# Performance work log

Hardware: AMD Instinct MI355X
Metric: run time of the kernel (lower is better)

## Reference

```python
import jax, jax.numpy as jnp
import numpy as np

B, T, C = 2, 2048, 1024
N = 16
D = C // N  # 64


def setup_inputs() -> dict:
    key = jax.random.key(0)
    ks = jax.random.split(key, 5)
    s = 1.0 / np.sqrt(C)  # lecun_normal-ish scale for Dense kernels
    return {
        "src": jax.random.normal(ks[0], (B, T, C), jnp.float32),
        "mask": jnp.ones((B, T), jnp.float32),  # unused on causal path
        "Wq": jax.random.normal(ks[1], (C, C), jnp.float32) * s,
        "bq": jnp.zeros((C,), jnp.float32),
        "Wk": jax.random.normal(ks[2], (C, C), jnp.float32) * s,
        "bk": jnp.zeros((C,), jnp.float32),
        "Wv": jax.random.normal(ks[3], (C, C), jnp.float32) * s,
        "bv": jnp.zeros((C,), jnp.float32),
        "Wo": jax.random.normal(ks[4], (C, C), jnp.float32) * s,
        "bo": jnp.zeros((C,), jnp.float32),
    }


def reference(src, mask, Wq, bq, Wk, bk, Wv, bv, Wo, bo):
    # QKV projections -> [B, N, T, D]
    def heads(x):
        return x.reshape(B, T, N, D).transpose(0, 2, 1, 3)

    q = heads(src @ Wq + bq)
    k = heads(src @ Wk + bk)
    v = heads(src @ Wv + bv)

    # scores [B, N, T, T], causal mask, softmax
    scores = jnp.einsum("bntd,bnsd->bnts", q, k) / jnp.sqrt(jnp.float32(D))
    causal = jnp.tril(jnp.ones((T, T), bool))
    scores = jnp.where(causal, scores, -jnp.inf)
    attn = jax.nn.softmax(scores, axis=-1)

    # weighted values, merge heads, output projection (dropout deterministic)
    out = jnp.einsum("bnts,bnsd->bntd", attn, v)
    out = out.transpose(0, 2, 1, 3).reshape(B, T, C)
    return out @ Wo + bo
```

## Files before the change

kernel.cpp:

```cpp
#include <hip/hip_runtime.h>

typedef __bf16 bf16;
typedef bf16 bf16x8 __attribute__((ext_vector_type(8)));
typedef float f32x4 __attribute__((ext_vector_type(4)));
typedef unsigned short u16;
typedef u16 u16x4 __attribute__((ext_vector_type(4)));

typedef const __attribute__((address_space(1))) void* gptr_t;
typedef __attribute__((address_space(3))) void* sptr_t;

__device__ __forceinline__ void async16(const void* g, void* l) {
  __builtin_amdgcn_global_load_lds((gptr_t)g, (sptr_t)l, 16, 0, 0);
}
__device__ __forceinline__ u16 f2bf(float v) {
  return __builtin_bit_cast(u16, (bf16)v);
}

__global__ void kPrep(const float* __restrict__ src, u16* __restrict__ Xs,
                      const float* __restrict__ Wq, const float* __restrict__ Wk,
                      const float* __restrict__ Wv, const float* __restrict__ Wo,
                      u16* __restrict__ Wt) {
  __shared__ float tile[32][33];
  const int bid = blockIdx.x, tid = threadIdx.x;
  if (bid < 4096) {
    const int i = (bid * 256 + tid) * 4;
    float4 v = *(const float4*)&src[i];
    u16x4 o = {f2bf(v.x), f2bf(v.y), f2bf(v.z), f2bf(v.w)};
    *(u16x4*)&Xs[i] = o;
  } else {
    const int t = bid - 4096;
    const int z = t >> 10, tt = t & 1023;
    const float* W = (z == 0) ? Wq : (z == 1) ? Wk : (z == 2) ? Wv : Wo;
    const int n0 = (tt & 31) * 32, k0 = (tt >> 5) * 32;
    const int tx = tid & 31, ty = tid >> 5;
#pragma unroll
    for (int j = 0; j < 4; ++j)
      tile[ty + j * 8][tx] = W[(size_t)(k0 + ty + j * 8) * 1024 + n0 + tx];
    __syncthreads();
#pragma unroll
    for (int j = 0; j < 4; ++j)
      Wt[(size_t)z * 1048576 + (size_t)(n0 + ty + j * 8) * 1024 + k0 + tx] =
          f2bf(tile[tx][ty + j * 8]);
  }
}

template <int EPI>
__global__ __launch_bounds__(256, 2) void kGemm(
    const u16* __restrict__ A, const u16* __restrict__ Bt,
    const float* __restrict__ b0, const float* __restrict__ b1,
    const float* __restrict__ b2, u16* __restrict__ outQ,
    float* __restrict__ outF) {
  __shared__ __align__(16) u16 As[2][128 * 32];
  __shared__ __align__(16) u16 Bs[2][128 * 32];
  const int tid = threadIdx.x, l = tid & 63, w = tid >> 6;
  const int bid = (blockIdx.x & 7) * (gridDim.x >> 3) + (blockIdx.x >> 3);
  const int mb = bid & 31, nb = bid >> 5;
  const int mbase = mb * 128, nbase = nb * 128;
  const int wr = (w >> 1) * 64, wc = (w & 1) * 64;
  f32x4 acc[4][4];
#pragma unroll
  for (int i = 0; i < 4; ++i)
#pragma unroll
    for (int j = 0; j < 4; ++j) acc[i][j] = (f32x4){0.f, 0.f, 0.f, 0.f};

  auto stage = [&](int bufi, int kt) {
#pragma unroll
    for (int i = 0; i < 2; ++i) {
      const int q = (w * 2 + i) * 64 + l;
      const int r = q >> 2, sl = q & 3;
      const int ksw = (sl ^ ((r >> 1) & 3)) * 8;
      async16(&A[(size_t)(mbase + r) * 1024 + kt * 32 + ksw],
              &As[bufi][(w * 2 + i) * 512]);
      async16(&Bt[(size_t)(nbase + r) * 1024 + kt * 32 + ksw],
              &Bs[bufi][(w * 2 + i) * 512]);
    }
  };

  stage(0, 0);
  for (int kt = 0; kt < 32; ++kt) {
    const int cur = kt & 1;
    if (kt < 31) {
      stage(cur ^ 1, kt + 1);
      asm volatile("s_waitcnt vmcnt(4)" ::: "memory");
    } else {
      asm volatile("s_waitcnt vmcnt(0)" ::: "memory");
    }
    __builtin_amdgcn_s_barrier();
    __builtin_amdgcn_sched_barrier(0);

    bf16x8 a[4], b[4];
#pragma unroll
    for (int mf = 0; mf < 4; ++mf) {
      const int row = wr + mf * 16 + (l & 15);
      const int slot = (l >> 4) ^ ((row >> 1) & 3);
      a[mf] = *(const bf16x8*)&As[cur][row * 32 + slot * 8];
    }
#pragma unroll
    for (int nf = 0; nf < 4; ++nf) {
      const int row = wc + nf * 16 + (l & 15);
      const int slot = (l >> 4) ^ ((row >> 1) & 3);
      b[nf] = *(const bf16x8*)&Bs[cur][row * 32 + slot * 8];
    }
#pragma unroll
    for (int mf = 0; mf < 4; ++mf)
#pragma unroll
      for (int nf = 0; nf < 4; ++nf)
        acc[mf][nf] = __builtin_amdgcn_mfma_f32_16x16x32_bf16(a[mf], b[nf],
                                                              acc[mf][nf], 0, 0, 0);
    __builtin_amdgcn_s_barrier();
  }

  if constexpr (EPI == 0) {
    const int mat = nb >> 3;
    const float* bias = (mat == 0) ? b0 : (mat == 1) ? b1 : b2;
    const float qscale = (mat == 0) ? 0.1803368801f : 1.0f;
    u16* Qo = outQ;
    u16* Ko = outQ + 4 * 1048576;
    u16* Vo = outQ + 8 * 1048576;
#pragma unroll
    for (int nf = 0; nf < 4; ++nf) {
      const int n = nbase + wc + nf * 16 + (l & 15);
      const int c = n & 1023, h = c >> 6, d = c & 63;
      const float bsv = bias[c];
#pragma unroll
      for (int mf = 0; mf < 4; ++mf)
#pragma unroll
        for (int r = 0; r < 4; ++r) {
          const int m = mbase + wr + mf * 16 + (l >> 4) * 4 + r;
          const int bb = m >> 11, t = m & 2047;
          const u16 hv = f2bf((acc[mf][nf][r] + bsv) * qscale);
          if (mat == 0)
            Qo[((size_t)(bb * 16 + h) * 2048 + t) * 64 + d] = hv;
          else if (mat == 1)
            Ko[((size_t)(bb * 16 + h) * 2048 + t) * 64 + d] = hv;
          else
            Vo[((size_t)(bb * 16 + h) * 64 + d) * 2048 + t] = hv;
        }
    }
  } else {
#pragma unroll
    for (int nf = 0; nf < 4; ++nf) {
      const int n = nbase + wc + nf * 16 + (l & 15);
      const float bsv = b0[n];
#pragma unroll
      for (int mf = 0; mf < 4; ++mf)
#pragma unroll
        for (int r = 0; r < 4; ++r) {
          const int m = mbase + wr + mf * 16 + (l >> 4) * 4 + r;
          outF[(size_t)m * 1024 + n] = acc[mf][nf][r] + bsv;
        }
    }
  }
}

#define PSTR 88
__global__ __launch_bounds__(256, 2) void kAttn(const u16* __restrict__ Q,
                                                const u16* __restrict__ K,
                                                const u16* __restrict__ Vt,
                                                u16* __restrict__ AO) {
  __shared__ __align__(16) u16 Ksh[2][64 * 64];
  __shared__ __align__(16) u16 Vsh[2][64 * 64];
  __shared__ __align__(16) u16 Pl[4][16 * PSTR];
  const int tid = threadIdx.x, l = tid & 63, w = tid >> 6;
  const int g = l >> 4, c = l & 15;
  const int pi = blockIdx.x, bh = blockIdx.y;
  const int qtA = pi, qtB = 31 - pi;
  const size_t head = (size_t)bh * 131072;

  bf16x8 aqA[2], aqB[2];
  {
    const int qrA = qtA * 64 + w * 16 + c;
    const int qrB = qtB * 64 + w * 16 + c;
#pragma unroll
    for (int ks = 0; ks < 2; ++ks) {
      aqA[ks] = *(const bf16x8*)&Q[head + (size_t)qrA * 64 + ks * 32 + g * 8];
      aqB[ks] = *(const bf16x8*)&Q[head + (size_t)qrB * 64 + ks * 32 + g * 8];
    }
  }

  f32x4 accA[4], accB[4];
#pragma unroll
  for (int i = 0; i < 4; ++i) {
    accA[i] = (f32x4){0.f, 0.f, 0.f, 0.f};
    accB[i] = (f32x4){0.f, 0.f, 0.f, 0.f};
  }
  float lA_ = 0.f, lB_ = 0.f;

  auto stage = [&](int bufi, int st) {
#pragma unroll
    for (int i = 0; i < 2; ++i) {
      const int q = (w * 2 + i) * 64 + l;
      const int r = q >> 3, sl = q & 7;
      const int ksw = (sl ^ (r & 7)) * 8;
      async16(&K[head + (size_t)(st * 64 + r) * 64 + ksw], &Ksh[bufi][(w * 2 + i) * 512]);
      async16(&Vt[head + (size_t)r * 2048 + st * 64 + ksw], &Vsh[bufi][(w * 2 + i) * 512]);
    }
  };

  auto computeTile = [&](int st, int qt, bf16x8* aq, f32x4* accO, float& lpart,
                         int cur) {
    f32x4 sT[4];
#pragma unroll
    for (int i = 0; i < 4; ++i) sT[i] = (f32x4){0.f, 0.f, 0.f, 0.f};
#pragma unroll
    for (int ks = 0; ks < 2; ++ks)
#pragma unroll
      for (int nf = 0; nf < 4; ++nf) {
        const int row = nf * 16 + c;
        const int slot = (ks * 4 + g) ^ (row & 7);
        bf16x8 bk = *(const bf16x8*)&Ksh[cur][row * 64 + slot * 8];
        sT[nf] = __builtin_amdgcn_mfma_f32_16x16x32_bf16(bk, aq[ks], sT[nf], 0, 0, 0);
      }

    float v[16];
#pragma unroll
    for (int nf = 0; nf < 4; ++nf)
#pragma unroll
      for (int r = 0; r < 4; ++r) v[nf * 4 + r] = sT[nf][r];
    if (st == qt) {
      const int qg = w * 16 + c;
#pragma unroll
      for (int nf = 0; nf < 4; ++nf)
#pragma unroll
        for (int r = 0; r < 4; ++r)
          if (nf * 16 + g * 4 + r > qg) v[nf * 4 + r] = -__builtin_inff();
    }

    float p[16];
#pragma unroll
    for (int i = 0; i < 16; ++i) p[i] = __builtin_exp2f(v[i]);
#pragma unroll
    for (int nf = 0; nf < 4; ++nf) {
      u16x4 q4 = {f2bf(p[nf * 4 + 0]), f2bf(p[nf * 4 + 1]),
                  f2bf(p[nf * 4 + 2]), f2bf(p[nf * 4 + 3])};
      *(u16x4*)&Pl[w][c * PSTR + nf * 16 + g * 4] = q4;
    }
    float s0 = (p[0] + p[1]) + (p[2] + p[3]);
    float s1 = (p[4] + p[5]) + (p[6] + p[7]);
    float s2 = (p[8] + p[9]) + (p[10] + p[11]);
    float s3 = (p[12] + p[13]) + (p[14] + p[15]);
    lpart += (s0 + s1) + (s2 + s3);

#pragma unroll
    for (int ks2 = 0; ks2 < 2; ++ks2) {
      bf16x8 pf = *(const bf16x8*)&Pl[w][c * PSTR + ks2 * 32 + g * 8];
#pragma unroll
      for (int nd = 0; nd < 4; ++nd) {
        const int row = nd * 16 + c;
        const int slot = (ks2 * 4 + g) ^ (row & 7);
        bf16x8 vf = *(const bf16x8*)&Vsh[cur][row * 64 + slot * 8];
        accO[nd] = __builtin_amdgcn_mfma_f32_16x16x32_bf16(pf, vf, accO[nd], 0, 0, 0);
      }
    }
  };

  stage(0, 0);
  for (int st = 0; st <= qtB; ++st) {
    const int cur = st & 1;
    if (st < qtB) {
      stage(cur ^ 1, st + 1);
      asm volatile("s_waitcnt vmcnt(4)" ::: "memory");
    } else {
      asm volatile("s_waitcnt vmcnt(0)" ::: "memory");
    }
    __builtin_amdgcn_s_barrier();
    __builtin_amdgcn_sched_barrier(0);

    computeTile(st, qtB, aqB, accB, lB_, cur);
    if (st <= qtA) computeTile(st, qtA, aqA, accA, lA_, cur);

    __builtin_amdgcn_s_barrier();
  }

  const int b = bh >> 4, h = bh & 15;
  auto writeOut = [&](int qt, f32x4* accO, float lpart) {
    float lc = lpart + __shfl_xor(lpart, 16);
    lc += __shfl_xor(lc, 32);
#pragma unroll
    for (int r = 0; r < 4; ++r) {
      const float lr = __shfl(lc, g * 4 + r);
      const float rin = 1.0f / lr;
      const int t = qt * 64 + w * 16 + g * 4 + r;
#pragma unroll
      for (int nd = 0; nd < 4; ++nd)
        AO[(size_t)(b * 2048 + t) * 1024 + h * 64 + nd * 16 + c] =
            f2bf(accO[nd][r] * rin);
    }
  };
  writeOut(qtA, accA, lA_);
  writeOut(qtB, accB, lB_);
}

extern "C" void kernel_launch(void* const* d_in, const int* in_sizes, int n_in,
                              void* d_out, int out_size, void* d_ws, size_t ws_size,
                              hipStream_t stream) {
  const float* src = (const float*)d_in[0];
  const float* Wq = (const float*)d_in[2];
  const float* bq = (const float*)d_in[3];
  const float* Wk = (const float*)d_in[4];
  const float* bk = (const float*)d_in[5];
  const float* Wv = (const float*)d_in[6];
  const float* bv = (const float*)d_in[7];
  const float* Wo = (const float*)d_in[8];
  const float* bo = (const float*)d_in[9];
  float* out = (float*)d_out;

  char* ws = (char*)d_ws;
  u16* Wt = (u16*)(ws);
  u16* Xs = (u16*)(ws + 8ull * 1024 * 1024);
  u16* Qb = (u16*)(ws + 16ull * 1024 * 1024);
  u16* AO = (u16*)(ws + 40ull * 1024 * 1024);

  kPrep<<<dim3(8192), dim3(256), 0, stream>>>(src, Xs, Wq, Wk, Wv, Wo, Wt);
  kGemm<0><<<dim3(32 * 24), dim3(256), 0, stream>>>(Xs, Wt, bq, bk, bv, Qb, nullptr);
  kAttn<<<dim3(16, 32), dim3(256), 0, stream>>>(Qb, Qb + 4 * 1048576,
                                                Qb + 8 * 1048576, AO);
  kGemm<1><<<dim3(32 * 8), dim3(256), 0, stream>>>(AO, Wt + 3ull * 1048576, bo,
                                                   nullptr, nullptr, nullptr, out);
}
```

Measured before the change: 127.6 us.

## Drop LDS staging in GEMMs and attention; load MFMA operands directly from global

```diff
diff --git a/kernel.cpp b/kernel.cpp
--- a/kernel.cpp
+++ b/kernel.cpp
@@ -6,12 +6,6 @@
 typedef unsigned short u16;
 typedef u16 u16x4 __attribute__((ext_vector_type(4)));
 
-typedef const __attribute__((address_space(1))) void* gptr_t;
-typedef __attribute__((address_space(3))) void* sptr_t;
-
-__device__ __forceinline__ void async16(const void* g, void* l) {
-  __builtin_amdgcn_global_load_lds((gptr_t)g, (sptr_t)l, 16, 0, 0);
-}
 __device__ __forceinline__ u16 f2bf(float v) {
   return __builtin_bit_cast(u16, (bf16)v);
 }
@@ -44,112 +38,126 @@
   }
 }
 
-template <int EPI>
-__global__ __launch_bounds__(256, 2) void kGemm(
+__global__ __launch_bounds__(256, 2) void kGemmQKV(
     const u16* __restrict__ A, const u16* __restrict__ Bt,
     const float* __restrict__ b0, const float* __restrict__ b1,
-    const float* __restrict__ b2, u16* __restrict__ outQ,
-    float* __restrict__ outF) {
-  __shared__ __align__(16) u16 As[2][128 * 32];
-  __shared__ __align__(16) u16 Bs[2][128 * 32];
+    const float* __restrict__ b2, u16* __restrict__ outQ) {
   const int tid = threadIdx.x, l = tid & 63, w = tid >> 6;
-  const int bid = (blockIdx.x & 7) * (gridDim.x >> 3) + (blockIdx.x >> 3);
+  const int bid = (blockIdx.x & 7) * 96 + (blockIdx.x >> 3);
   const int mb = bid & 31, nb = bid >> 5;
   const int mbase = mb * 128, nbase = nb * 128;
   const int wr = (w >> 1) * 64, wc = (w & 1) * 64;
+  const int hi = l >> 4, lo = l & 15;
+
+  const u16* abase[4];
+  const u16* bbase[4];
+#pragma unroll
+  for (int mf = 0; mf < 4; ++mf)
+    abase[mf] = &A[(size_t)(mbase + wr + mf * 16 + lo) * 1024 + hi * 8];
+#pragma unroll
+  for (int nf = 0; nf < 4; ++nf)
+    bbase[nf] = &Bt[(size_t)(nbase + wc + nf * 16 + lo) * 1024 + hi * 8];
+
   f32x4 acc[4][4];
 #pragma unroll
   for (int i = 0; i < 4; ++i)
 #pragma unroll
     for (int j = 0; j < 4; ++j) acc[i][j] = (f32x4){0.f, 0.f, 0.f, 0.f};
 
-  auto stage = [&](int bufi, int kt) {
-#pragma unroll
-    for (int i = 0; i < 2; ++i) {
-      const int q = (w * 2 + i) * 64 + l;
-      const int r = q >> 2, sl = q & 3;
-      const int ksw = (sl ^ ((r >> 1) & 3)) * 8;
-      async16(&A[(size_t)(mbase + r) * 1024 + kt * 32 + ksw],
-              &As[bufi][(w * 2 + i) * 512]);
-      async16(&Bt[(size_t)(nbase + r) * 1024 + kt * 32 + ksw],
-              &Bs[bufi][(w * 2 + i) * 512]);
-    }
-  };
-
-  stage(0, 0);
+#pragma unroll 2
   for (int kt = 0; kt < 32; ++kt) {
-    const int cur = kt & 1;
-    if (kt < 31) {
-      stage(cur ^ 1, kt + 1);
-      asm volatile("s_waitcnt vmcnt(4)" ::: "memory");
-    } else {
-      asm volatile("s_waitcnt vmcnt(0)" ::: "memory");
-    }
-    __builtin_amdgcn_s_barrier();
-    __builtin_amdgcn_sched_barrier(0);
-
     bf16x8 a[4], b[4];
 #pragma unroll
-    for (int mf = 0; mf < 4; ++mf) {
-      const int row = wr + mf * 16 + (l & 15);
-      const int slot = (l >> 4) ^ ((row >> 1) & 3);
-      a[mf] = *(const bf16x8*)&As[cur][row * 32 + slot * 8];
-    }
-#pragma unroll
-    for (int nf = 0; nf < 4; ++nf) {
-      const int row = wc + nf * 16 + (l & 15);
-      const int slot = (l >> 4) ^ ((row >> 1) & 3);
-      b[nf] = *(const bf16x8*)&Bs[cur][row * 32 + slot * 8];
-    }
+    for (int mf = 0; mf < 4; ++mf) a[mf] = *(const bf16x8*)&abase[mf][kt * 32];
+#pragma unroll
+    for (int nf = 0; nf < 4; ++nf) b[nf] = *(const bf16x8*)&bbase[nf][kt * 32];
 #pragma unroll
     for (int mf = 0; mf < 4; ++mf)
 #pragma unroll
       for (int nf = 0; nf < 4; ++nf)
         acc[mf][nf] = __builtin_amdgcn_mfma_f32_16x16x32_bf16(a[mf], b[nf],
                                                               acc[mf][nf], 0, 0, 0);
-    __builtin_amdgcn_s_barrier();
-  }
-
-  if constexpr (EPI == 0) {
-    const int mat = nb >> 3;
-    const float* bias = (mat == 0) ? b0 : (mat == 1) ? b1 : b2;
-    const float qscale = (mat == 0) ? 0.1803368801f : 1.0f;
-    u16* Qo = outQ;
-    u16* Ko = outQ + 4 * 1048576;
-    u16* Vo = outQ + 8 * 1048576;
-#pragma unroll
-    for (int nf = 0; nf < 4; ++nf) {
-      const int n = nbase + wc + nf * 16 + (l & 15);
-      const int c = n & 1023, h = c >> 6, d = c & 63;
-      const float bsv = bias[c];
-#pragma unroll
-      for (int mf = 0; mf < 4; ++mf)
-#pragma unroll
-        for (int r = 0; r < 4; ++r) {
-          const int m = mbase + wr + mf * 16 + (l >> 4) * 4 + r;
-          const int bb = m >> 11, t = m & 2047;
-          const u16 hv = f2bf((acc[mf][nf][r] + bsv) * qscale);
-          if (mat == 0)
-            Qo[((size_t)(bb * 16 + h) * 2048 + t) * 64 + d] = hv;
-          else if (mat == 1)
-            Ko[((size_t)(bb * 16 + h) * 2048 + t) * 64 + d] = hv;
-          else
-            Vo[((size_t)(bb * 16 + h) * 64 + d) * 2048 + t] = hv;
-        }
-    }
-  } else {
-#pragma unroll
-    for (int nf = 0; nf < 4; ++nf) {
-      const int n = nbase + wc + nf * 16 + (l & 15);
-      const float bsv = b0[n];
-#pragma unroll
-      for (int mf = 0; mf < 4; ++mf)
-#pragma unroll
-        for (int r = 0; r < 4; ++r) {
-          const int m = mbase + wr + mf * 16 + (l >> 4) * 4 + r;
-          outF[(size_t)m * 1024 + n] = acc[mf][nf][r] + bsv;
-        }
-    }
+  }
+
+  u16* Qo = outQ;
+  u16* Ko = outQ + 4 * 1048576;
+  u16* Vo = outQ + 8 * 1048576;
+  const int mat = nb >> 3;
+  const float* bias = (mat == 0) ? b0 : (mat == 1) ? b1 : b2;
+  const float qs = (mat == 0) ? 0.1803368801f : 1.0f;
+#pragma unroll
+  for (int nf = 0; nf < 4; ++nf) {
+    const int n = nbase + wc + nf * 16 + lo;
+    const int cc = n & 1023, h = cc >> 6, d = cc & 63;
+    const float bsv = bias[cc];
+#pragma unroll
+    for (int mf = 0; mf < 4; ++mf)
+#pragma unroll
+      for (int r = 0; r < 4; ++r) {
+        const int m = mbase + wr + mf * 16 + hi * 4 + r;
+        const int bb = m >> 11, t = m & 2047;
+        const u16 hv = f2bf((acc[mf][nf][r] + bsv) * qs);
+        if (mat == 0)
+          Qo[((size_t)(bb * 16 + h) * 2048 + t) * 64 + d] = hv;
+        else if (mat == 1)
+          Ko[((size_t)(bb * 16 + h) * 2048 + t) * 64 + d] = hv;
+        else
+          Vo[((size_t)(bb * 16 + h) * 64 + d) * 2048 + t] = hv;
+      }
+  }
+}
+
+__global__ __launch_bounds__(256, 2) void kGemmO(
+    const u16* __restrict__ A, const u16* __restrict__ Bt,
+    const float* __restrict__ b0, float* __restrict__ outF) {
+  const int tid = threadIdx.x, l = tid & 63, w = tid >> 6;
+  const int bid = (blockIdx.x & 7) * 64 + (blockIdx.x >> 3);
+  const int mb = bid & 31, nb = bid >> 5;
+  const int mbase = mb * 128, nbase = nb * 64;
+  const int wr = (w >> 1) * 64, wc = (w & 1) * 32;
+  const int hi = l >> 4, lo = l & 15;
+
+  const u16* abase[4];
+  const u16* bbase[2];
+#pragma unroll
+  for (int mf = 0; mf < 4; ++mf)
+    abase[mf] = &A[(size_t)(mbase + wr + mf * 16 + lo) * 1024 + hi * 8];
+#pragma unroll
+  for (int nf = 0; nf < 2; ++nf)
+    bbase[nf] = &Bt[(size_t)(nbase + wc + nf * 16 + lo) * 1024 + hi * 8];
+
+  f32x4 acc[4][2];
+#pragma unroll
+  for (int i = 0; i < 4; ++i)
+#pragma unroll
+    for (int j = 0; j < 2; ++j) acc[i][j] = (f32x4){0.f, 0.f, 0.f, 0.f};
+
+#pragma unroll 2
+  for (int kt = 0; kt < 32; ++kt) {
+    bf16x8 a[4], b[2];
+#pragma unroll
+    for (int mf = 0; mf < 4; ++mf) a[mf] = *(const bf16x8*)&abase[mf][kt * 32];
+#pragma unroll
+    for (int nf = 0; nf < 2; ++nf) b[nf] = *(const bf16x8*)&bbase[nf][kt * 32];
+#pragma unroll
+    for (int mf = 0; mf < 4; ++mf)
+#pragma unroll
+      for (int nf = 0; nf < 2; ++nf)
+        acc[mf][nf] = __builtin_amdgcn_mfma_f32_16x16x32_bf16(a[mf], b[nf],
+                                                              acc[mf][nf], 0, 0, 0);
+  }
+
+#pragma unroll
+  for (int nf = 0; nf < 2; ++nf) {
+    const int n = nbase + wc + nf * 16 + lo;
+    const float bsv = b0[n];
+#pragma unroll
+    for (int mf = 0; mf < 4; ++mf)
+#pragma unroll
+      for (int r = 0; r < 4; ++r) {
+        const int m = mbase + wr + mf * 16 + hi * 4 + r;
+        outF[(size_t)m * 1024 + n] = acc[mf][nf][r] + bsv;
+      }
   }
 }
 
@@ -158,14 +166,14 @@
                                                 const u16* __restrict__ K,
                                                 const u16* __restrict__ Vt,
                                                 u16* __restrict__ AO) {
-  __shared__ __align__(16) u16 Ksh[2][64 * 64];
-  __shared__ __align__(16) u16 Vsh[2][64 * 64];
   __shared__ __align__(16) u16 Pl[4][16 * PSTR];
   const int tid = threadIdx.x, l = tid & 63, w = tid >> 6;
   const int g = l >> 4, c = l & 15;
   const int pi = blockIdx.x, bh = blockIdx.y;
   const int qtA = pi, qtB = 31 - pi;
   const size_t head = (size_t)bh * 131072;
+  const u16* Kh = K + head;
+  const u16* Vh = Vt + head;
 
   bf16x8 aqA[2], aqB[2];
   {
@@ -186,19 +194,7 @@
   }
   float lA_ = 0.f, lB_ = 0.f;
 
-  auto stage = [&](int bufi, int st) {
-#pragma unroll
-    for (int i = 0; i < 2; ++i) {
-      const int q = (w * 2 + i) * 64 + l;
-      const int r = q >> 3, sl = q & 7;
-      const int ksw = (sl ^ (r & 7)) * 8;
-      async16(&K[head + (size_t)(st * 64 + r) * 64 + ksw], &Ksh[bufi][(w * 2 + i) * 512]);
-      async16(&Vt[head + (size_t)r * 2048 + st * 64 + ksw], &Vsh[bufi][(w * 2 + i) * 512]);
-    }
-  };
-
-  auto computeTile = [&](int st, int qt, bf16x8* aq, f32x4* accO, float& lpart,
-                         int cur) {
+  auto computeTile = [&](int st, int qt, bf16x8* aq, f32x4* accO, float& lpart) {
     f32x4 sT[4];
 #pragma unroll
     for (int i = 0; i < 4; ++i) sT[i] = (f32x4){0.f, 0.f, 0.f, 0.f};
@@ -206,9 +202,8 @@
     for (int ks = 0; ks < 2; ++ks)
 #pragma unroll
       for (int nf = 0; nf < 4; ++nf) {
-        const int row = nf * 16 + c;
-        const int slot = (ks * 4 + g) ^ (row & 7);
-        bf16x8 bk = *(const bf16x8*)&Ksh[cur][row * 64 + slot * 8];
+        bf16x8 bk = *(const bf16x8*)&Kh[(size_t)(st * 64 + nf * 16 + c) * 64 +
+                                        ks * 32 + g * 8];
         sT[nf] = __builtin_amdgcn_mfma_f32_16x16x32_bf16(bk, aq[ks], sT[nf], 0, 0, 0);
       }
 
@@ -246,30 +241,17 @@
       bf16x8 pf = *(const bf16x8*)&Pl[w][c * PSTR + ks2 * 32 + g * 8];
 #pragma unroll
       for (int nd = 0; nd < 4; ++nd) {
-        const int row = nd * 16 + c;
-        const int slot = (ks2 * 4 + g) ^ (row & 7);
-        bf16x8 vf = *(const bf16x8*)&Vsh[cur][row * 64 + slot * 8];
+        bf16x8 vf = *(const bf16x8*)&Vh[(size_t)(nd * 16 + c) * 2048 + st * 64 +
+                                        ks2 * 32 + g * 8];
         accO[nd] = __builtin_amdgcn_mfma_f32_16x16x32_bf16(pf, vf, accO[nd], 0, 0, 0);
       }
     }
   };
 
-  stage(0, 0);
+#pragma unroll 2
   for (int st = 0; st <= qtB; ++st) {
-    const int cur = st & 1;
-    if (st < qtB) {
-      stage(cur ^ 1, st + 1);
-      asm volatile("s_waitcnt vmcnt(4)" ::: "memory");
-    } else {
-      asm volatile("s_waitcnt vmcnt(0)" ::: "memory");
-    }
-    __builtin_amdgcn_s_barrier();
-    __builtin_amdgcn_sched_barrier(0);
-
-    computeTile(st, qtB, aqB, accB, lB_, cur);
-    if (st <= qtA) computeTile(st, qtA, aqA, accA, lA_, cur);
-
-    __builtin_amdgcn_s_barrier();
+    computeTile(st, qtB, aqB, accB, lB_);
+    if (st <= qtA) computeTile(st, qtA, aqA, accA, lA_);
   }
 
   const int b = bh >> 4, h = bh & 15;
@@ -312,9 +294,8 @@
   u16* AO = (u16*)(ws + 40ull * 1024 * 1024);
 
   kPrep<<<dim3(8192), dim3(256), 0, stream>>>(src, Xs, Wq, Wk, Wv, Wo, Wt);
-  kGemm<0><<<dim3(32 * 24), dim3(256), 0, stream>>>(Xs, Wt, bq, bk, bv, Qb, nullptr);
+  kGemmQKV<<<dim3(768), dim3(256), 0, stream>>>(Xs, Wt, bq, bk, bv, Qb);
   kAttn<<<dim3(16, 32), dim3(256), 0, stream>>>(Qb, Qb + 4 * 1048576,
                                                 Qb + 8 * 1048576, AO);
-  kGemm<1><<<dim3(32 * 8), dim3(256), 0, stream>>>(AO, Wt + 3ull * 1048576, bo,
-                                                   nullptr, nullptr, nullptr, out);
-}
+  kGemmO<<<dim3(512), dim3(256), 0, stream>>>(AO, Wt + 3ull * 1048576, bo, out);
+}
```

After: 283.4 us. +122.1%, slower.
